# Kernel tuning notes

Measured on AMD Instinct MI355X. Metric: run time of the kernel, lower is better.

Reference implementation:

```python
import jax, jax.numpy as jnp
import numpy as np

D_MODEL = 256
N_HEADS = 8
HEAD_DIM = D_MODEL // N_HEADS


def setup_inputs() -> dict:
    key = jax.random.key(0)
    ks = jax.random.split(key, 10)
    B, L, D = 2, 2048, D_MODEL
    s = 1.0 / np.sqrt(D)
    inp = {
        "x": jax.random.normal(ks[0], (B, L, D), dtype=jnp.float32),
        "Wq": jax.random.normal(ks[1], (D, D), dtype=jnp.float32) * s,
        "bq": jnp.zeros((D,), jnp.float32),
        "Wk": jax.random.normal(ks[2], (D, D), dtype=jnp.float32) * s,
        "bk": jnp.zeros((D,), jnp.float32),
        "Wv": jax.random.normal(ks[3], (D, D), dtype=jnp.float32) * s,
        "bv": jnp.zeros((D,), jnp.float32),
        "u": jax.random.normal(ks[4], (N_HEADS, 1, 1), dtype=jnp.float32) * 0.1,
        "Wo": jax.random.normal(ks[5], (D, D), dtype=jnp.float32) * s,
        "bo": jnp.zeros((D,), jnp.float32),
    }
    return inp


def reference(x, Wq, bq, Wk, bk, Wv, bv, u, Wo, bo):
    B, L, D = x.shape
    H, hd = N_HEADS, HEAD_DIM

    def proj(W, b):  # torch Linear: x @ W.T + b -> [B,H,L,hd]
        return (x @ W.T + b).reshape(B, L, H, hd).transpose(0, 2, 1, 3)

    Q, K, V = proj(Wq, bq), proj(Wk, bk), proj(Wv, bv)

    scores = jnp.einsum("bhqd,bhkd->bhqk", Q, K) / np.sqrt(hd)
    attn_series = jax.nn.softmax(scores, axis=-1)  # [B,H,L,L]

    pos = jnp.arange(L, dtype=jnp.float32)
    dist = jnp.abs(pos[None, :] - pos[:, None])  # [L,L]
    # prior per head: exp(-d^2 / (2*(u^2+1e-6))), normalized over last dim
    prior = jnp.exp(-(dist[None] ** 2) / (2.0 * (u ** 2 + 1e-6)))  # [H,L,L]
    prior = prior / (prior.sum(axis=-1, keepdims=True) + 1e-6)

    discrepancy = jnp.abs(attn_series - prior[None]).mean(axis=(1, 2))  # [B,L]

    out = jnp.einsum("bhqk,bhkd->bhqd", attn_series, V)
    out = out.transpose(0, 2, 1, 3).reshape(B, L, D)
    out = out @ Wo.T + bo
    return out, discrepancy
```

## Files before the change

kernel.cpp:

```cpp
#include <hip/hip_runtime.h>
#include <hip/hip_bf16.h>
#include <math.h>

#define LSEQ 2048
#define DMODEL 256
#define NH 8
#define HD 32

typedef __attribute__((ext_vector_type(8))) short bf16x8;
typedef __attribute__((ext_vector_type(4))) float f32x4;

#define MFMA __builtin_amdgcn_mfma_f32_16x16x32_bf16

__device__ __forceinline__ short f2bf(float x) {
  __hip_bfloat16 h = __float2bfloat16(x);
  return __builtin_bit_cast(short, h);
}
__device__ __forceinline__ float bf2f(short s) {
  __hip_bfloat16 h = __builtin_bit_cast(__hip_bfloat16, s);
  return __bfloat162float(h);
}
__device__ __forceinline__ short bftrunc(float x) {
  return (short)(__builtin_bit_cast(unsigned int, x) >> 16);
}
__device__ __forceinline__ float fexp2(float x) {
#if __has_builtin(__builtin_amdgcn_exp2f)
  return __builtin_amdgcn_exp2f(x);
#else
  return __expf(x * 0.6931471805599453f);
#endif
}

__global__ __launch_bounds__(256) void aux_kernel(
    const float* __restrict__ x,
    const float* __restrict__ Wq, const float* __restrict__ Wk,
    const float* __restrict__ Wv, const float* __restrict__ Wo,
    const float* __restrict__ u,
    short* __restrict__ xh,
    short* __restrict__ Wh,
    short* __restrict__ Woh, short* __restrict__ Wol,
    float* __restrict__ Eb, float* __restrict__ Zb)
{
  __shared__ float Cs[LSEQ];
  __shared__ float part[256];
  const int tid = threadIdx.x;
  if (blockIdx.x < 1024) {
    const int i4 = (blockIdx.x * 256 + tid) * 4;
    float4 v = *(const float4*)(x + i4);
    *(short4*)(xh + i4) = make_short4(f2bf(v.x), f2bf(v.y), f2bf(v.z), f2bf(v.w));
    return;
  }
  const int bx = blockIdx.x - 1024;
  if (bx < 256) {
    const int i4 = (bx * 256 + tid) * 4;
    if (i4 < 196608) {
      int row = i4 >> 8, col = i4 & 255;
      const float* W = (row < 256) ? Wq : (row < 512) ? Wk : Wv;
      float4 v = *(const float4*)(W + (row & 255) * 256 + col);
      *(short4*)(Wh + i4) = make_short4(f2bf(v.x), f2bf(v.y), f2bf(v.z), f2bf(v.w));
    } else {
      int j = i4 - 196608;
      float4 v = *(const float4*)(Wo + j);
      short h0 = f2bf(v.x), h1 = f2bf(v.y), h2 = f2bf(v.z), h3 = f2bf(v.w);
      *(short4*)(Woh + j) = make_short4(h0, h1, h2, h3);
      *(short4*)(Wol + j) = make_short4(bftrunc(v.x - bf2f(h0)), bftrunc(v.y - bf2f(h1)),
                                        bftrunc(v.z - bf2f(h2)), bftrunc(v.w - bf2f(h3)));
    }
    return;
  }
  const int h = bx - 256;
  const float uu = u[h];
  const float den = 2.0f * (uu * uu + 1e-6f);
  float e[8]; float run = 0.f;
  const int base = tid * 8;
#pragma unroll
  for (int j = 0; j < 8; ++j) {
    float d = (float)(base + j);
    e[j] = __expf(-(d * d) / den);
    run += e[j];
  }
  part[tid] = run;
  __syncthreads();
  for (int off = 1; off < 256; off <<= 1) {
    float v = (tid >= off) ? part[tid - off] : 0.f;
    __syncthreads();
    part[tid] += v;
    __syncthreads();
  }
  float c = part[tid] - run;
#pragma unroll
  for (int j = 0; j < 8; ++j) {
    c += e[j];
    Cs[base + j] = c;
    Eb[h * LSEQ + base + j] = e[j];
  }
  __syncthreads();
  const float E0 = Cs[0];
  for (int i = tid; i < LSEQ; i += 256) {
    float s = Cs[i] + Cs[LSEQ - 1 - i] - E0;
    Zb[h * LSEQ + i] = 1.0f / (s + 1e-6f);
  }
}

__global__ __launch_bounds__(256) void qkv_gemm(
    const short* __restrict__ xh,
    const short* __restrict__ Bh,
    const float* __restrict__ bq, const float* __restrict__ bk,
    const float* __restrict__ bv,
    short* __restrict__ Qf, short* __restrict__ Kf, short* __restrict__ Vf)
{
  const int tid = threadIdx.x, w = tid >> 6, lane = tid & 63;
  const int l15 = lane & 15, q4 = lane >> 4;
  const int m0 = blockIdx.x * 64, n0 = blockIdx.y * 64;
  const int mrow = m0 + w * 16 + l15;
  f32x4 acc[4] = {{0,0,0,0},{0,0,0,0},{0,0,0,0},{0,0,0,0}};
  for (int k0 = 0; k0 < 256; k0 += 32) {
    bf16x8 ah = *(const bf16x8*)&xh[(size_t)mrow * 256 + k0 + q4 * 8];
#pragma unroll
    for (int nt = 0; nt < 4; ++nt) {
      const size_t bi = (size_t)(n0 + nt * 16 + l15) * 256 + k0 + q4 * 8;
      bf16x8 bh = *(const bf16x8*)&Bh[bi];
      acc[nt] = MFMA(ah, bh, acc[nt], 0, 0, 0);
    }
  }
  const int type = n0 >> 8;
  const int n0l = n0 & 255;
  const float* bias = (type == 0) ? bq : (type == 1) ? bk : bv;
  const float qls = 0.25503489f;
#pragma unroll
  for (int nt = 0; nt < 4; ++nt) {
    const int col = n0l + nt * 16 + l15;
    const float bvv = bias[col];
    const int hh = col >> 5, dloc = col & 31;
#pragma unroll
    for (int r = 0; r < 4; ++r) {
      const int m = m0 + w * 16 + q4 * 4 + r;
      float v = acc[nt][r] + bvv;
      const int bb = m >> 11, mm = m & 2047, rr = mm & 15;
      if (type == 2) {
        const int kt128 = mm >> 7, low7 = mm & 127;
        const int wv = (low7 >> 4) & 3, ph = low7 >> 6;
        const int c = ph * 16 + rr;
        const size_t idx =
          ((((((size_t)bb * 8 + hh) * 16 + kt128) * 4 + wv) * 2 + (dloc >> 4)) * 64
           + (c >> 3) * 16 + (dloc & 15)) * 8 + (c & 7);
        Vf[idx] = f2bf(v);
      } else if (type == 0) {
        const int qblk = mm >> 5, rg = (mm >> 4) & 1;
        const size_t idx =
          (((((size_t)bb * 8 + hh) * 64 + qblk) * 2 + rg) * 64
           + (dloc >> 3) * 16 + rr) * 8 + (dloc & 7);
        Qf[idx] = f2bf(v * qls);
      } else {
        const int g = mm >> 4;
        const size_t idx =
          ((((size_t)bb * 8 + hh) * 128 + g) * 64
           + (dloc >> 3) * 16 + rr) * 8 + (dloc & 7);
        Kf[idx] = f2bf(v);
      }
    }
  }
}

__global__ __launch_bounds__(512, 4) void attn_kernel(
    const short* __restrict__ Qf, const short* __restrict__ Kf,
    const short* __restrict__ Vf,
    const float* __restrict__ Eb, const float* __restrict__ Zb,
    short* __restrict__ Ohb, short* __restrict__ Olb,
    short* __restrict__ Dp)
{
  __shared__ short Pp[16 * 2048];
  __shared__ float Elds[192];
  __shared__ float lpart[8][16];
  __shared__ float lpn[16];
  __shared__ float liz[16];

  const int tid = threadIdx.x, w = tid >> 6, lane = tid & 63;
  const int l15 = lane & 15, q4 = lane >> 4;
  const int flat = blockIdx.x + 128 * (blockIdx.y + 8 * blockIdx.z);
  const int slot = flat >> 3;
  const int g = (flat & 7) | ((slot >> 7) << 3);
  const int h = g & 7, b = g >> 3;
  const int qslot = slot & 127, q0 = qslot * 16;
  const int bh = b * NH + h;

  if (tid < 192) Elds[tid] = Eb[h * LSEQ + tid];
  if (tid < 16)  liz[tid] = Zb[h * LSEQ + q0 + tid];

  const bf16x8* Qf8 = (const bf16x8*)Qf;
  const bf16x8* Kf8 = (const bf16x8*)Kf;
  const bf16x8* Vf8 = (const bf16x8*)Vf;

  bf16x8 qh = Qf8[((size_t)bh * 128 + qslot) * 64 + lane];

  const size_t kfb = (size_t)bh * 128;
  const size_t vfb = (size_t)bh * 16;
  const int wv = w & 3, wh = w >> 2;

  float lac[4] = {0.f, 0.f, 0.f, 0.f};
#pragma unroll 2
  for (int it = 0; it < 8; ++it) {
    const int g16 = it * 16 + wh * 8 + wv;
    bf16x8 k0 = Kf8[(kfb + g16) * 64 + lane];
    bf16x8 k1 = Kf8[(kfb + g16 + 4) * 64 + lane];
    f32x4 s0 = {0.f,0.f,0.f,0.f}; s0 = MFMA(qh, k0, s0, 0, 0, 0);
    f32x4 s1 = {0.f,0.f,0.f,0.f}; s1 = MFMA(qh, k1, s1, 0, 0, 0);
    const int cc0 = it * 256 + w * 32 + l15;
#pragma unroll
    for (int r = 0; r < 4; ++r) {
      const int row = q4 * 4 + r;
      const int sw = (row & 7) << 3;
      float p0 = fexp2(s0[r]);
      float p1 = fexp2(s1[r]);
      lac[r] += p0 + p1;
      Pp[(row * 2048 + cc0) ^ sw]      = bftrunc(p0);
      Pp[(row * 2048 + cc0 + 16) ^ sw] = bftrunc(p1);
    }
  }
#pragma unroll
  for (int r = 0; r < 4; ++r) {
    float v = lac[r];
    v += __shfl_xor(v, 1); v += __shfl_xor(v, 2);
    v += __shfl_xor(v, 4); v += __shfl_xor(v, 8);
    if (l15 == 0) lpart[w][q4 * 4 + r] = v;
  }
  __syncthreads();
  if (tid < 16) {
    float l = 0.f;
#pragma unroll
    for (int w8 = 0; w8 < 8; ++w8) l += lpart[w8][tid];
    lpn[tid] = 1.0f / l;
  }
  __syncthreads();

  float pn4[4], iz4[4];
#pragma unroll
  for (int r = 0; r < 4; ++r) {
    pn4[r] = lpn[q4 * 4 + r];
    iz4[r] = liz[q4 * 4 + r];
  }

  const size_t drow = (size_t)(g * 128 + qslot) * LSEQ;
  f32x4 oacc[2] = {{0,0,0,0},{0,0,0,0}};
#pragma unroll 2
  for (int it = 0; it < 8; ++it) {
    const int kt128 = it * 2 + wh;
    bf16x8 vb0 = Vf8[(((vfb + kt128) * 4 + wv) * 2 + 0) * 64 + lane];
    bf16x8 vb1 = Vf8[(((vfb + kt128) * 4 + wv) * 2 + 1) * 64 + lane];
#pragma unroll
    for (int ph = 0; ph < 2; ++ph) {
      const int c0g = kt128 * 128 + ph * 64 + wv * 16;
      const int kg = c0g + l15;
      const int dd = c0g - q0;
      const bool near = (dd >= -96) && (dd <= 96);
      const int ccd = it * 256 + w * 32 + ph * 16 + l15;
      float dsum = 0.f;
#pragma unroll
      for (int r = 0; r < 4; ++r) {
        const int row = q4 * 4 + r;
        float p = bf2f(Pp[(row * 2048 + ccd) ^ ((row & 7) << 3)]) * pn4[r];
        if (near) {
          int qrow = q0 + row;
          int dist = (qrow >= kg) ? (qrow - kg) : (kg - qrow);
          dsum += fabsf(p - Elds[dist] * iz4[r]);
        } else {
          dsum += p;
        }
      }
      dsum += __shfl_xor(dsum, 16);
      dsum += __shfl_xor(dsum, 32);
      if (q4 == 0) Dp[drow + kg] = f2bf(dsum);
    }
    const int cp = it * 256 + w * 32 + q4 * 8;
    bf16x8 pa = *(const bf16x8*)&Pp[(l15 * 2048 + cp) ^ ((l15 & 7) << 3)];
    oacc[0] = MFMA(pa, vb0, oacc[0], 0, 0, 0);
    oacc[1] = MFMA(pa, vb1, oacc[1], 0, 0, 0);
  }

  __syncthreads();
  float* Ored = (float*)Pp;
#pragma unroll
  for (int dt = 0; dt < 2; ++dt) {
#pragma unroll
    for (int r = 0; r < 4; ++r)
      Ored[(w * 16 + q4 * 4 + r) * 17 + l15] = oacc[dt][r];
    __syncthreads();
    if (tid < 256) {
      const int q = tid >> 4, d = tid & 15;
      float v = 0.f;
#pragma unroll
      for (int w8 = 0; w8 < 8; ++w8) v += Ored[(w8 * 16 + q) * 17 + d];
      v *= lpn[q];
      const size_t oo = ((size_t)b * LSEQ + q0 + q) * DMODEL + h * HD + dt * 16 + d;
      short hi = f2bf(v);
      Ohb[oo] = hi;
      Olb[oo] = bftrunc(v - bf2f(hi));
    }
    __syncthreads();
  }
}

__global__ __launch_bounds__(256) void tail_kernel(
    const short* __restrict__ Ah, const short* __restrict__ Al,
    const short* __restrict__ Bh, const short* __restrict__ Bl,
    const float* __restrict__ bias, float* __restrict__ C,
    const short* __restrict__ Dp, float* __restrict__ disc)
{
  __shared__ float red[8][33];
  const int tid = threadIdx.x;
  if (blockIdx.x < 512) {
    const int w = tid >> 6, lane = tid & 63;
    const int l15 = lane & 15, q4 = lane >> 4;
    const int m0 = (blockIdx.x & 63) * 64, n0 = (blockIdx.x >> 6) * 32;
    const int mrow = m0 + w * 16 + l15;
    f32x4 acc[2] = {{0,0,0,0},{0,0,0,0}};
    for (int k0 = 0; k0 < 256; k0 += 32) {
      bf16x8 ah = *(const bf16x8*)&Ah[(size_t)mrow * 256 + k0 + q4 * 8];
      bf16x8 al = *(const bf16x8*)&Al[(size_t)mrow * 256 + k0 + q4 * 8];
#pragma unroll
      for (int nt = 0; nt < 2; ++nt) {
        const size_t bi = (size_t)(n0 + nt * 16 + l15) * 256 + k0 + q4 * 8;
        bf16x8 bh = *(const bf16x8*)&Bh[bi];
        bf16x8 bl = *(const bf16x8*)&Bl[bi];
        acc[nt] = MFMA(ah, bh, acc[nt], 0, 0, 0);
        acc[nt] = MFMA(al, bh, acc[nt], 0, 0, 0);
        acc[nt] = MFMA(ah, bl, acc[nt], 0, 0, 0);
      }
    }
#pragma unroll
    for (int nt = 0; nt < 2; ++nt) {
      const int col = n0 + nt * 16 + l15;
      const float bvv = bias[col];
#pragma unroll
      for (int r = 0; r < 4; ++r) {
        const int m = m0 + w * 16 + q4 * 4 + r;
        C[(size_t)m * 256 + col] = acc[nt][r] + bvv;
      }
    }
    return;
  }
  const int bid = blockIdx.x - 512;
  const int b = bid >> 6, kb = (bid & 63) * 32;
  const int k = kb + (tid & 31), sg = tid >> 5;
  float acc = 0.f;
  const short* base = Dp + ((size_t)b * 1024 + (size_t)sg * 128) * LSEQ + k;
#pragma unroll 4
  for (int i = 0; i < 128; ++i) acc += bf2f(base[(size_t)i * LSEQ]);
  red[sg][tid & 31] = acc;
  __syncthreads();
  if (tid < 32) {
    float v = 0.f;
#pragma unroll
    for (int s2 = 0; s2 < 8; ++s2) v += red[s2][tid];
    disc[b * LSEQ + kb + tid] = v * (1.0f / ((float)NH * (float)LSEQ));
  }
}

extern "C" void kernel_launch(void* const* d_in, const int* in_sizes, int n_in,
                              void* d_out, int out_size, void* d_ws, size_t ws_size,
                              hipStream_t stream)
{
  const float* x  = (const float*)d_in[0];
  const float* Wq = (const float*)d_in[1];
  const float* bq = (const float*)d_in[2];
  const float* Wk = (const float*)d_in[3];
  const float* bk = (const float*)d_in[4];
  const float* Wv = (const float*)d_in[5];
  const float* bv = (const float*)d_in[6];
  const float* u  = (const float*)d_in[7];
  const float* Wo = (const float*)d_in[8];
  const float* bo = (const float*)d_in[9];

  float* out  = (float*)d_out;
  float* disc = out + (size_t)2 * LSEQ * DMODEL;

  char* w8 = (char*)d_ws;
  const size_t MB = 1u << 20;
  short* Qfb = (short*)(w8);
  short* Kfb = (short*)(w8 + 2 * MB);
  short* Vfb = (short*)(w8 + 4 * MB);
  short* Ohb = (short*)(w8 + 6 * MB);
  short* Olb = (short*)(w8 + 8 * MB);
  short* Wh  = (short*)(w8 + 10 * MB);
  short* Woh = (short*)(w8 + 10 * MB + 393216);
  short* Wol = (short*)(w8 + 10 * MB + 524288);
  float* Eb  = (float*)(w8 + 11 * MB);
  float* Zb  = (float*)(w8 + 11 * MB + 65536);
  short* xh  = (short*)(w8 + 12 * MB);
  short* Dp  = (short*)(w8 + 14 * MB);

  aux_kernel<<<1288, 256, 0, stream>>>(x, Wq, Wk, Wv, Wo, u, xh, Wh, Woh, Wol, Eb, Zb);
  qkv_gemm<<<dim3(64, 12), 256, 0, stream>>>(xh, Wh, bq, bk, bv, Qfb, Kfb, Vfb);
  attn_kernel<<<dim3(128, 8, 2), 512, 0, stream>>>(Qfb, Kfb, Vfb, Eb, Zb,
                                                   Ohb, Olb, Dp);
  tail_kernel<<<640, 256, 0, stream>>>(Ohb, Olb, Woh, Wol, bo, out, Dp, disc);
}
```

Baseline: 165.4 us.

## Fuse PV MFMA into score loop and keep probabilities in registers

Drops the 64KB shared buffer that held the full 16x2048 probability tile. The P·V MFMA now runs inside the score loop through a small per-wave transpose buffer, and the bf16 probabilities are kept packed in registers for the later discrepancy pass. The goal is to raise occupancy by cutting LDS use and to remove the second pass of LDS reads. In exchange it costs about 32 more VGPRs per thread, and probabilities are now rounded to bf16 instead of truncated.

```diff
diff --git a/kernel.cpp b/kernel.cpp
--- a/kernel.cpp
+++ b/kernel.cpp
@@ -169,7 +169,7 @@
     short* __restrict__ Ohb, short* __restrict__ Olb,
     short* __restrict__ Dp)
 {
-  __shared__ short Pp[16 * 2048];
+  __shared__ short Pt[8][16][40];
   __shared__ float Elds[192];
   __shared__ float lpart[8][16];
   __shared__ float lpn[16];
@@ -197,26 +197,40 @@
   const size_t vfb = (size_t)bh * 16;
   const int wv = w & 3, wh = w >> 2;
 
+  unsigned int pc[8][4];
   float lac[4] = {0.f, 0.f, 0.f, 0.f};
-#pragma unroll 2
+  f32x4 oacc[2] = {{0,0,0,0},{0,0,0,0}};
+
+#pragma unroll
   for (int it = 0; it < 8; ++it) {
     const int g16 = it * 16 + wh * 8 + wv;
     bf16x8 k0 = Kf8[(kfb + g16) * 64 + lane];
     bf16x8 k1 = Kf8[(kfb + g16 + 4) * 64 + lane];
+    const int kt128 = it * 2 + wh;
+    bf16x8 vb0 = Vf8[(((vfb + kt128) * 4 + wv) * 2 + 0) * 64 + lane];
+    bf16x8 vb1 = Vf8[(((vfb + kt128) * 4 + wv) * 2 + 1) * 64 + lane];
     f32x4 s0 = {0.f,0.f,0.f,0.f}; s0 = MFMA(qh, k0, s0, 0, 0, 0);
     f32x4 s1 = {0.f,0.f,0.f,0.f}; s1 = MFMA(qh, k1, s1, 0, 0, 0);
-    const int cc0 = it * 256 + w * 32 + l15;
+    short c0[4], c1[4];
 #pragma unroll
     for (int r = 0; r < 4; ++r) {
-      const int row = q4 * 4 + r;
-      const int sw = (row & 7) << 3;
       float p0 = fexp2(s0[r]);
       float p1 = fexp2(s1[r]);
       lac[r] += p0 + p1;
-      Pp[(row * 2048 + cc0) ^ sw]      = bftrunc(p0);
-      Pp[(row * 2048 + cc0 + 16) ^ sw] = bftrunc(p1);
-    }
-  }
+      c0[r] = f2bf(p0);
+      c1[r] = f2bf(p1);
+      Pt[w][q4 * 4 + r][l15]      = c0[r];
+      Pt[w][q4 * 4 + r][16 + l15] = c1[r];
+    }
+    pc[it][0] = (unsigned int)(unsigned short)c0[0] | ((unsigned int)(unsigned short)c0[1] << 16);
+    pc[it][1] = (unsigned int)(unsigned short)c0[2] | ((unsigned int)(unsigned short)c0[3] << 16);
+    pc[it][2] = (unsigned int)(unsigned short)c1[0] | ((unsigned int)(unsigned short)c1[1] << 16);
+    pc[it][3] = (unsigned int)(unsigned short)c1[2] | ((unsigned int)(unsigned short)c1[3] << 16);
+    bf16x8 pa = *(const bf16x8*)&Pt[w][l15][q4 * 8];
+    oacc[0] = MFMA(pa, vb0, oacc[0], 0, 0, 0);
+    oacc[1] = MFMA(pa, vb1, oacc[1], 0, 0, 0);
+  }
+
 #pragma unroll
   for (int r = 0; r < 4; ++r) {
     float v = lac[r];
@@ -239,46 +253,44 @@
     pn4[r] = lpn[q4 * 4 + r];
     iz4[r] = liz[q4 * 4 + r];
   }
+  const int qrow0 = q0 + q4 * 4;
 
   const size_t drow = (size_t)(g * 128 + qslot) * LSEQ;
-  f32x4 oacc[2] = {{0,0,0,0},{0,0,0,0}};
-#pragma unroll 2
+#pragma unroll
   for (int it = 0; it < 8; ++it) {
-    const int kt128 = it * 2 + wh;
-    bf16x8 vb0 = Vf8[(((vfb + kt128) * 4 + wv) * 2 + 0) * 64 + lane];
-    bf16x8 vb1 = Vf8[(((vfb + kt128) * 4 + wv) * 2 + 1) * 64 + lane];
 #pragma unroll
     for (int ph = 0; ph < 2; ++ph) {
-      const int c0g = kt128 * 128 + ph * 64 + wv * 16;
+      const int c0g = (it * 2 + wh) * 128 + ph * 64 + wv * 16;
       const int kg = c0g + l15;
       const int dd = c0g - q0;
       const bool near = (dd >= -96) && (dd <= 96);
-      const int ccd = it * 256 + w * 32 + ph * 16 + l15;
+      const unsigned int wlo = pc[it][ph * 2 + 0];
+      const unsigned int whi = pc[it][ph * 2 + 1];
+      float pr[4];
+      pr[0] = __builtin_bit_cast(float, wlo << 16);
+      pr[1] = __builtin_bit_cast(float, wlo & 0xffff0000u);
+      pr[2] = __builtin_bit_cast(float, whi << 16);
+      pr[3] = __builtin_bit_cast(float, whi & 0xffff0000u);
       float dsum = 0.f;
-#pragma unroll
-      for (int r = 0; r < 4; ++r) {
-        const int row = q4 * 4 + r;
-        float p = bf2f(Pp[(row * 2048 + ccd) ^ ((row & 7) << 3)]) * pn4[r];
-        if (near) {
-          int qrow = q0 + row;
+      if (near) {
+#pragma unroll
+        for (int r = 0; r < 4; ++r) {
+          float p = pr[r] * pn4[r];
+          int qrow = qrow0 + r;
           int dist = (qrow >= kg) ? (qrow - kg) : (kg - qrow);
           dsum += fabsf(p - Elds[dist] * iz4[r]);
-        } else {
-          dsum += p;
         }
+      } else {
+        dsum = pr[0] * pn4[0] + pr[1] * pn4[1] + pr[2] * pn4[2] + pr[3] * pn4[3];
       }
       dsum += __shfl_xor(dsum, 16);
       dsum += __shfl_xor(dsum, 32);
       if (q4 == 0) Dp[drow + kg] = f2bf(dsum);
     }
-    const int cp = it * 256 + w * 32 + q4 * 8;
-    bf16x8 pa = *(const bf16x8*)&Pp[(l15 * 2048 + cp) ^ ((l15 & 7) << 3)];
-    oacc[0] = MFMA(pa, vb0, oacc[0], 0, 0, 0);
-    oacc[1] = MFMA(pa, vb1, oacc[1], 0, 0, 0);
-  }
-
-  __syncthreads();
-  float* Ored = (float*)Pp;
+  }
+
+  __syncthreads();
+  float* Ored = (float*)Pt;
 #pragma unroll
   for (int dt = 0; dt < 2; ++dt) {
 #pragma unroll
```

Result: faster. 159.9 us (-3.3%).
